# Kernel optimization log

Measured on AMD Instinct MI355X. Metric: run time of the kernel, lower is better.

Reference implementation:

```python
import jax, jax.numpy as jnp
import numpy as np

B, C, H, W = 2, 96, 40, 40
DIN, N, R, K = 192, 16, 6, 4  # d_inner, d_state, dt_rank, k_group


def silu(x):
    return x * jax.nn.sigmoid(x)


def dwconv3x3(x, w, b):
    # depthwise 3x3, SAME padding; w: (DIN,1,3,3)
    y = jax.lax.conv_general_dilated(x, w, (1, 1), [(1, 1), (1, 1)],
                                     feature_group_count=x.shape[1])
    return y + b[None, :, None, None]


def cross_scan(x):
    # (B,C,H,W) -> (B,4,C,L): row-major, col-major, and their reverses
    b, c, h, w = x.shape
    x0 = x.reshape(b, c, h * w)
    x1 = x.transpose(0, 1, 3, 2).reshape(b, c, h * w)
    return jnp.stack([x0, x1, x0[..., ::-1], x1[..., ::-1]], axis=1)


def cross_merge(y, h, w):
    # (B,4,C,H,W) -> (B,C,L)
    b, k, c = y.shape[0], y.shape[1], y.shape[2]
    y = y.reshape(b, k, c, h * w)
    y = y[:, :2] + y[:, 2:][..., ::-1]
    y1 = y[:, 1].reshape(b, c, w, h).transpose(0, 1, 3, 2).reshape(b, c, h * w)
    return y[:, 0] + y1


def selective_scan(u, dt, A, Bm, Cm, Dv, dbias):
    # u, dt: (B,K,DIN,L); A: (K*DIN,N); Bm, Cm: (B,K,N,L); Dv: (K*DIN,); dbias: (K*DIN,)
    b, k, d, l = u.shape
    n = A.shape[1]
    A4 = A.reshape(k, d, n)
    dt = jax.nn.softplus(dt + dbias.reshape(1, k, d, 1))
    # discretize: dA = exp(dt*A), dBu = dt*B*u  -> shapes (B,K,D,L,N)
    dA = jnp.exp(dt[..., None] * A4[None, :, :, None, :])
    dBu = dt[..., None] * Bm.transpose(0, 1, 3, 2)[:, :, None, :, :] * u[..., None]

    def combine(c1, c2):
        a1, b1 = c1
        a2, b2 = c2
        return a1 * a2, a2 * b1 + b2

    _, h = jax.lax.associative_scan(combine, (dA, dBu), axis=3)  # h: (B,K,D,L,N)
    y = jnp.einsum('bkdln,bknl->bkdl', h, Cm)
    return y + Dv.reshape(1, k, d, 1) * u


def ln2d(x, g, b):
    # LayerNorm over channel dim (channel_first LayerNorm2d)
    mu = x.mean(axis=1, keepdims=True)
    var = jnp.mean((x - mu) ** 2, axis=1, keepdims=True)
    xn = (x - mu) / jnp.sqrt(var + 1e-5)
    return xn * g[None, :, None, None] + b[None, :, None, None]


def setup_inputs():
    key = jax.random.key(0)
    ks = jax.random.split(key, 24)

    def rn(k, shape, s=0.02):
        return jax.random.normal(k, shape, dtype=jnp.float32) * s

    A_log = jnp.tile(jnp.log(jnp.arange(1, N + 1, dtype=jnp.float32))[None, :], (K * DIN, 1))
    return {
        'x_rgb': jax.random.normal(ks[0], (B, C, H, W), jnp.float32),
        'x_e': jax.random.normal(ks[1], (B, C, H, W), jnp.float32),
        'in_proj_w': rn(ks[2], (DIN, C)),
        'in_proj_mx_w': rn(ks[3], (DIN, C)),
        'conv_w': rn(ks[4], (DIN, 1, 3, 3), 0.1),
        'conv_b': jnp.zeros((DIN,), jnp.float32),
        'xproj1_w': rn(ks[5], (K, R + 2 * N, DIN)),
        'xproj2_w': rn(ks[6], (K, R + 2 * N, DIN)),
        'dtproj1_w': rn(ks[7], (K, DIN, R), 0.1),
        'dtproj1_b': rn(ks[8], (K, DIN), 0.1) - 4.0,
        'dtproj2_w': rn(ks[9], (K, DIN, R), 0.1),
        'dtproj2_b': rn(ks[10], (K, DIN), 0.1) - 4.0,
        'A_log_1': A_log,
        'A_log_2': A_log,
        'D_1': jnp.ones((K * DIN,), jnp.float32),
        'D_2': jnp.ones((K * DIN,), jnp.float32),
        'norm1_g': jnp.ones((DIN,), jnp.float32),
        'norm1_b': jnp.zeros((DIN,), jnp.float32),
        'norm2_g': jnp.ones((DIN,), jnp.float32),
        'norm2_b': jnp.zeros((DIN,), jnp.float32),
        'fc1_w1': rn(ks[11], (DIN // 16, DIN), 0.05),
        'fc1_w2': rn(ks[12], (DIN, DIN // 16), 0.05),
        'fc2_w1': rn(ks[13], (DIN // 16, DIN), 0.05),
        'fc2_w2': rn(ks[14], (DIN, DIN // 16), 0.05),
        'out_proj_w': rn(ks[15], (C, 2 * DIN)),
    }


def reference(x_rgb, x_e, in_proj_w, in_proj_mx_w, conv_w, conv_b, xproj1_w, xproj2_w,
              dtproj1_w, dtproj1_b, dtproj2_w, dtproj2_b, A_log_1, A_log_2, D_1, D_2,
              norm1_g, norm1_b, norm2_g, norm2_b, fc1_w1, fc1_w2, fc2_w1, fc2_w2, out_proj_w):
    # in_proj (1x1 conv style Linear2d)
    xr = jnp.einsum('oc,bchw->bohw', in_proj_w, x_rgb)
    xe = jnp.einsum('oc,bchw->bohw', in_proj_mx_w, x_e)
    # shared depthwise conv + SiLU
    xr = silu(dwconv3x3(xr, conv_w, conv_b))
    xe = silu(dwconv3x3(xe, conv_w, conv_b))
    b, d, h, w = xr.shape

    xs_r = cross_scan(xr)  # (B,K,DIN,L)
    xs_e = cross_scan(xe)

    def proj(xs, xp_w, dt_w):
        t = jnp.einsum('bkdl,kcd->bkcl', xs, xp_w)  # grouped 1x1 conv1d
        dts, Bm, Cm = jnp.split(t, [R, R + N], axis=2)
        dts = jnp.einsum('bkrl,kdr->bkdl', dts, dt_w)
        return dts, Bm, Cm

    d_r, B_r, C_r = proj(xs_r, xproj1_w, dtproj1_w)
    d_e, B_e, C_e = proj(xs_e, xproj2_w, dtproj2_w)

    # cross attention: rgb scan consumes C and D of the other modality
    y_r = selective_scan(xs_r, d_r, -jnp.exp(A_log_1), B_r, C_e, D_2, dtproj1_b.reshape(-1))
    y_e = selective_scan(xs_e, d_e, -jnp.exp(A_log_2), B_e, C_r, D_1, dtproj2_b.reshape(-1))

    y_r = cross_merge(y_r.reshape(b, K, d, h, w), h, w).reshape(b, d, h, w)
    y_e = cross_merge(y_e.reshape(b, K, d, h, w), h, w).reshape(b, d, h, w)
    y_r = ln2d(y_r, norm1_g, norm1_b)
    y_e = ln2d(y_e, norm2_g, norm2_b)

    # cross squeeze-excitation
    sq_r = xr.mean(axis=(2, 3))
    sq_e = xe.mean(axis=(2, 3))
    exc_r = jax.nn.sigmoid(silu(sq_r @ fc1_w1.T) @ fc1_w2.T)
    exc_e = jax.nn.sigmoid(silu(sq_e @ fc2_w1.T) @ fc2_w2.T)
    y_r = y_r * exc_e[:, :, None, None]
    y_e = y_e * exc_r[:, :, None, None]

    y = jnp.concatenate([y_r, y_e], axis=1)  # (B, 2*DIN, H, W)
    return jnp.einsum('oc,bchw->bohw', out_proj_w, y)
```

## Files before the change

kernel.cpp:

```cpp
#include <hip/hip_runtime.h>
#include <math.h>

#define BN   2
#define CIN  96
#define HH   40
#define WW   40
#define LL   1600
#define DIN  192
#define NS   16
#define RR   6
#define KK   4
#define CH   25

typedef _Float16 h16;

__device__ __forceinline__ float sigmoidf_(float x){ return 1.0f/(1.0f+expf(-x)); }
__device__ __forceinline__ float softplus_fast(float x){
  return x > 20.0f ? x : __logf(1.0f + __expf(x));
}

__device__ __forceinline__ void pow_tree(float R, float* p){
  float R2 = R * R;
  float R4 = R2 * R2;
  float R8 = R4 * R4;
  p[0]  = R;        p[1]  = R2;       p[2]  = R2 * R;   p[3]  = R4;
  p[4]  = R4 * R;   p[5]  = R4 * R2;  p[6]  = R4 * p[2];p[7]  = R8;
  p[8]  = R8 * R;   p[9]  = R8 * R2;  p[10] = R8 * p[2];p[11] = R8 * R4;
  p[12] = R8 * p[4];p[13] = R8 * p[5];p[14] = R8 * p[6];p[15] = R8 * R8;
}

__device__ __forceinline__ void unpack8(float4 v, float* dst){
  const h16* hp = reinterpret_cast<const h16*>(&v);
  #pragma unroll
  for (int i = 0; i < 8; ++i) dst[i] = (float)hp[i];
}

__global__ void k_inproj(const float* __restrict__ x_rgb, const float* __restrict__ x_e,
                         const float* __restrict__ w_rgb, const float* __restrict__ w_e,
                         float* __restrict__ xproj){
  __shared__ float xin[16][100];
  int l0 = blockIdx.x * 16;
  int mb = blockIdx.y;
  int m = mb / BN, b = mb % BN;
  const float* xsrc = (m == 0 ? x_rgb : x_e) + (size_t)b * CIN * LL;
  const float* w    = (m == 0 ? w_rgb : w_e);
  for (int idx = threadIdx.x; idx < CIN * 16; idx += 256){
    int c = idx >> 4, px = idx & 15;
    xin[px][c] = xsrc[c * LL + l0 + px];
  }
  __syncthreads();
  int px = threadIdx.x & 15;
  int o0 = (threadIdx.x >> 4) * 12;
  float acc[12];
  #pragma unroll
  for (int i = 0; i < 12; ++i) acc[i] = 0.f;
  const float4* xv = reinterpret_cast<const float4*>(xin[px]);
  for (int cc = 0; cc < CIN / 4; ++cc){
    float4 x4 = xv[cc];
    #pragma unroll
    for (int i = 0; i < 12; ++i){
      float4 w4 = *reinterpret_cast<const float4*>(w + (o0 + i) * CIN + cc * 4);
      acc[i] += w4.x * x4.x + w4.y * x4.y + w4.z * x4.z + w4.w * x4.w;
    }
  }
  #pragma unroll
  for (int i = 0; i < 12; ++i)
    xproj[((size_t)mb * DIN + o0 + i) * LL + l0 + px] = acc[i];
}

__global__ void k_conv(const float* __restrict__ xproj, const float* __restrict__ conv_w,
                       const float* __restrict__ conv_b, h16* __restrict__ x_act,
                       h16* __restrict__ x_actT, h16* __restrict__ u_chA,
                       h16* __restrict__ u_chT, float* __restrict__ sq){
  __shared__ float pl[LL];
  __shared__ float sact[LL + HH];
  __shared__ float red[4];
  int d  = blockIdx.x;
  int mb = blockIdx.y;
  const float* src = xproj + ((size_t)mb * DIN + d) * LL;
  for (int p = threadIdx.x; p < LL; p += blockDim.x) pl[p] = src[p];
  __syncthreads();
  float cw[9];
  #pragma unroll
  for (int j = 0; j < 9; ++j) cw[j] = conv_w[d * 9 + j];
  float bias = conv_b[d];
  h16* dst = x_act + ((size_t)mb * DIN + d) * LL;
  float lsum = 0.f;
  for (int p = threadIdx.x; p < LL; p += blockDim.x){
    int py = p / WW, px = p % WW;
    float acc = bias;
    #pragma unroll
    for (int dy = -1; dy <= 1; ++dy){
      int yy = py + dy;
      if (yy < 0 || yy >= HH) continue;
      #pragma unroll
      for (int dx = -1; dx <= 1; ++dx){
        int xx = px + dx;
        if (xx < 0 || xx >= WW) continue;
        acc += cw[(dy + 1) * 3 + (dx + 1)] * pl[yy * WW + xx];
      }
    }
    float s = acc * sigmoidf_(acc);
    dst[p] = (h16)s;
    sact[p + p / WW] = s;
    lsum += s;
  }
  #pragma unroll
  for (int off = 32; off; off >>= 1) lsum += __shfl_down(lsum, off);
  if ((threadIdx.x & 63) == 0) red[threadIdx.x >> 6] = lsum;
  __syncthreads();
  if (threadIdx.x == 0)
    sq[mb * DIN + d] = (red[0] + red[1] + red[2] + red[3]) * (1.0f / LL);
  size_t po = ((size_t)mb * DIN + d) * LL;
  h16* dstT = x_actT + po;
  h16* uA   = u_chA + po;
  h16* uT   = u_chT + po;
  for (int q = threadIdx.x; q < LL; q += blockDim.x){
    int lt = (q % WW) * WW + q / WW;
    dstT[q] = (h16)sact[lt + lt / WW];
    int l = (q & 63) * CH + (q >> 6);
    uA[q] = (h16)sact[l + l / WW];
    int pt = (l % WW) * WW + l / WW;
    uT[q] = (h16)sact[pt + pt / WW];
  }
}

__global__ void k_xproj(const h16* __restrict__ x_act, const h16* __restrict__ x_actT,
                        const float* __restrict__ xp1, const float* __restrict__ xp2,
                        float* __restrict__ tdt_ch, h16* __restrict__ B_ch,
                        h16* __restrict__ C_ch){
  int l0 = blockIdx.x * 64;
  int k  = blockIdx.y;
  int mb = blockIdx.z; int m = mb / BN;
  const float* xw = (m == 0 ? xp1 : xp2) + k * 38 * DIN;
  const h16* xa = ((k & 1) ? x_actT : x_act) + (size_t)mb * DIN * LL;
  bool rev = (k >= 2);
  int ll = threadIdx.x & 63;
  int g  = threadIdx.x >> 6;
  int c0 = g * 10;
  int l  = l0 + ll; if (rev) l = LL - 1 - l;
  const h16* xcol = xa + l;
  float acc[10];
  #pragma unroll
  for (int i = 0; i < 10; ++i) acc[i] = 0.f;
  if (g < 3){
    for (int dd = 0; dd < DIN; ++dd){
      float xv = (float)xcol[(size_t)dd * LL];
      #pragma unroll
      for (int i = 0; i < 10; ++i) acc[i] += xw[(c0 + i) * DIN + dd] * xv;
    }
  } else {
    for (int dd = 0; dd < DIN; ++dd){
      float xv = (float)xcol[(size_t)dd * LL];
      #pragma unroll
      for (int i = 0; i < 8; ++i) acc[i] += xw[(c0 + i) * DIN + dd] * xv;
    }
  }
  int mbk = mb * KK + k;
  int lq = l0 + ll;
  int q = (lq % CH) * 64 + lq / CH;
  int nc = (g < 3) ? 10 : 8;
  for (int i = 0; i < nc; ++i){
    int c = c0 + i;
    float v = acc[i];
    if (c < RR){
      tdt_ch[((size_t)mbk * RR + c) * LL + q] = v;
    } else if (c < RR + NS){
      int n = c - RR;
      B_ch[(((size_t)mbk * 2 + (n >> 3)) * LL + q) * 8 + (n & 7)] = (h16)v;
    } else {
      int n = c - RR - NS;
      C_ch[(((size_t)mbk * 2 + (n >> 3)) * LL + q) * 8 + (n & 7)] = (h16)v;
    }
  }
}

__global__ void __launch_bounds__(256, 4) k_scan(
    const h16* __restrict__ u_chA, const h16* __restrict__ u_chT,
    const float* __restrict__ tdt_all, const h16* __restrict__ B_ch,
    const h16* __restrict__ C_ch,
    const float* __restrict__ Alog1, const float* __restrict__ Alog2,
    const float* __restrict__ D1, const float* __restrict__ D2,
    const float* __restrict__ dtw1, const float* __restrict__ dtb1,
    const float* __restrict__ dtw2, const float* __restrict__ dtb2,
    h16* __restrict__ y_px){
  __shared__ h16 ysth[4][LL];
  __shared__ float dt_lds[4][LL];
  int wv   = threadIdx.x >> 6;
  int lane = threadIdx.x & 63;
  int chain = blockIdx.x * 4 + wv;
  int d   = chain % DIN;
  int mbk = chain / DIN;
  int k   = mbk % KK;
  int mb  = mbk / KK;
  int m = mb / BN, b = mb % BN;
  int kd = k * DIN + d;
  bool rev = (k >= 2);

  const float* Alog = (m == 0 ? Alog1 : Alog2) + kd * NS;
  float An[NS];
  bool fastA = true;
  #pragma unroll
  for (int n = 0; n < NS; ++n){
    An[n] = -__expf(Alog[n]);
    fastA = fastA && (fabsf(An[n] + (float)(n + 1)) <= 1e-4f * (float)(n + 1));
  }
  float Dv = (m == 0 ? D2 : D1)[kd];
  const float* dtw = (m == 0 ? dtw1 : dtw2) + kd * RR;
  float w0 = dtw[0], w1 = dtw[1], w2 = dtw[2], w3 = dtw[3], w4 = dtw[4], w5 = dtw[5];
  float dbias = (m == 0 ? dtb1 : dtb2)[kd];

  const float* t0 = tdt_all + (size_t)mbk * RR * LL;
  for (int s = 0; s < CH; ++s){
    int q = s * 64 + lane;
    float dtpre = w0 * t0[q] + w1 * t0[LL + q] + w2 * t0[2 * LL + q]
                + w3 * t0[3 * LL + q] + w4 * t0[4 * LL + q] + w5 * t0[5 * LL + q] + dbias;
    dt_lds[wv][q] = softplus_fast(dtpre);
  }

  const float4* B0 = reinterpret_cast<const float4*>(B_ch) + (size_t)mbk * 2 * LL;
  int mbk_o = ((1 - m) * BN + b) * KK + k;
  const float4* C0 = reinterpret_cast<const float4*>(C_ch) + (size_t)mbk_o * 2 * LL;
  const h16* urow = ((k & 1) ? u_chT : u_chA) + ((size_t)mb * DIN + d) * LL;

  float h[NS];
  #pragma unroll
  for (int n = 0; n < NS; ++n) h[n] = 0.f;
  float Sdt = 0.f;

  if (fastA){
    float4 bP0, bP1, cP0, cP1; float uP, dtP;
    {
      int q0 = lane;
      dtP = dt_lds[wv][q0];
      uP  = (float)urow[rev ? (LL - 1 - q0) : q0];
      bP0 = B0[q0]; bP1 = B0[LL + q0];
      cP0 = C0[q0]; cP1 = C0[LL + q0];
    }
    #pragma unroll 5
    for (int s = 0; s < CH; ++s){
      float dt = dtP, u = uP;
      float4 b0 = bP0, b1 = bP1, c0 = cP0, c1 = cP1;
      if (s + 1 < CH){
        int q1 = (s + 1) * 64 + lane;
        dtP = dt_lds[wv][q1];
        uP  = (float)urow[rev ? (LL - 1 - q1) : q1];
        bP0 = B0[q1]; bP1 = B0[LL + q1];
        cP0 = C0[q1]; cP1 = C0[LL + q1];
      }
      Sdt += dt;
      float du = dt * u;
      float Bv[NS], Cv[NS];
      unpack8(b0, Bv); unpack8(b1, Bv + 8);
      unpack8(c0, Cv); unpack8(c1, Cv + 8);
      float p[NS];
      pow_tree(__expf(-dt), p);
      float y0 = Dv * u, y1 = 0.f, y2 = 0.f, y3 = 0.f;
      #pragma unroll
      for (int n = 0; n < NS; ++n){
        h[n] = p[n] * h[n] + du * Bv[n];
        float t = h[n] * Cv[n];
        if      ((n & 3) == 0) y0 += t;
        else if ((n & 3) == 1) y1 += t;
        else if ((n & 3) == 2) y2 += t;
        else                   y3 += t;
      }
      ysth[wv][lane * CH + s] = (h16)((y0 + y1) + (y2 + y3));
    }
  } else {
    #pragma unroll 5
    for (int s = 0; s < CH; ++s){
      int q = s * 64 + lane;
      float dt = dt_lds[wv][q];
      Sdt += dt;
      float u  = (float)urow[rev ? (LL - 1 - q) : q];
      float du = dt * u;
      float Bv[NS], Cv[NS];
      unpack8(B0[q], Bv); unpack8(B0[LL + q], Bv + 8);
      unpack8(C0[q], Cv); unpack8(C0[LL + q], Cv + 8);
      float y0 = Dv * u, y1 = 0.f, y2 = 0.f, y3 = 0.f;
      #pragma unroll
      for (int n = 0; n < NS; ++n){
        float dA = __expf(dt * An[n]);
        h[n] = dA * h[n] + du * Bv[n];
        float t = h[n] * Cv[n];
        if      ((n & 3) == 0) y0 += t;
        else if ((n & 3) == 1) y1 += t;
        else if ((n & 3) == 2) y2 += t;
        else                   y3 += t;
      }
      ysth[wv][lane * CH + s] = (h16)((y0 + y1) + (y2 + y3));
    }
  }
  float aP[NS];
  if (fastA){
    pow_tree(__expf(-Sdt), aP);
  } else {
    #pragma unroll
    for (int n = 0; n < NS; ++n) aP[n] = __expf(Sdt * An[n]);
  }

  #pragma unroll
  for (int off = 1; off < 64; off <<= 1){
    #pragma unroll
    for (int n = 0; n < NS; ++n){
      float ap = __shfl_up(aP[n], off);
      float bp = __shfl_up(h[n],  off);
      if (lane >= off){
        h[n]  = aP[n] * bp + h[n];
        aP[n] = aP[n] * ap;
      }
    }
  }
  #pragma unroll
  for (int n = 0; n < NS; ++n){
    float v = __shfl_up(h[n], 1);
    h[n] = (lane == 0) ? 0.f : v;
  }

  if (fastA){
    float4 cP0, cP1; float dtP;
    {
      int q0 = lane;
      dtP = dt_lds[wv][q0];
      cP0 = C0[q0]; cP1 = C0[LL + q0];
    }
    float cum = 0.f;
    #pragma unroll 5
    for (int s = 0; s < CH; ++s){
      float dt = dtP;
      float4 c0 = cP0, c1 = cP1;
      if (s + 1 < CH){
        int q1 = (s + 1) * 64 + lane;
        dtP = dt_lds[wv][q1];
        cP0 = C0[q1]; cP1 = C0[LL + q1];
      }
      cum += dt;
      float Rc = __expf(-cum);
      float Cv[NS];
      unpack8(c0, Cv); unpack8(c1, Cv + 8);
      float p[NS];
      pow_tree(Rc, p);
      float s0 = 0.f, s1 = 0.f, s2 = 0.f, s3 = 0.f;
      #pragma unroll
      for (int n = 0; n < NS; ++n){
        float t = h[n] * p[n] * Cv[n];
        if      ((n & 3) == 0) s0 += t;
        else if ((n & 3) == 1) s1 += t;
        else if ((n & 3) == 2) s2 += t;
        else                   s3 += t;
      }
      int li = lane * CH + s;
      ysth[wv][li] = (h16)((float)ysth[wv][li] + (s0 + s1) + (s2 + s3));
    }
  } else {
    float cum = 0.f;
    #pragma unroll 5
    for (int s = 0; s < CH; ++s){
      int q = s * 64 + lane;
      cum += dt_lds[wv][q];
      float Cv[NS];
      unpack8(C0[q], Cv); unpack8(C0[LL + q], Cv + 8);
      float s0 = 0.f, s1 = 0.f, s2 = 0.f, s3 = 0.f;
      #pragma unroll
      for (int n = 0; n < NS; ++n){
        float t = h[n] * __expf(cum * An[n]) * Cv[n];
        if      ((n & 3) == 0) s0 += t;
        else if ((n & 3) == 1) s1 += t;
        else if ((n & 3) == 2) s2 += t;
        else                   s3 += t;
      }
      int li = lane * CH + s;
      ysth[wv][li] = (h16)((float)ysth[wv][li] + (s0 + s1) + (s2 + s3));
    }
  }

  h16* yo = y_px + (size_t)chain * LL;
  for (int qq = lane; qq < LL; qq += 64){
    int l;
    if      (k == 0) l = qq;
    else if (k == 1) l = (qq % WW) * WW + qq / WW;
    else if (k == 2) l = LL - 1 - qq;
    else             { int qt = (qq % WW) * WW + qq / WW; l = LL - 1 - qt; }
    yo[qq] = ysth[wv][l];
  }
}

__global__ void __launch_bounds__(256) k_mergeout(
    const h16* __restrict__ y_px, const float* __restrict__ sq,
    const float* __restrict__ fc1_w1, const float* __restrict__ fc1_w2,
    const float* __restrict__ fc2_w1, const float* __restrict__ fc2_w2,
    const float* __restrict__ n1g, const float* __restrict__ n1b,
    const float* __restrict__ n2g, const float* __restrict__ n2b,
    const float* __restrict__ wout, float* __restrict__ out){
  __shared__ float acc[2 * DIN][9];
  __shared__ float yt[8][388];
  __shared__ float ps[2][8][16], ps2[2][8][16];
  __shared__ float mu_s[2][8], inv_s[2][8];
  __shared__ float sqs[2][DIN];
  __shared__ float hid[2][12];
  __shared__ float exc_s[2][DIN];
  int p0 = blockIdx.x * 8;
  int b  = blockIdx.y;
  int tid = threadIdx.x;
  for (int idx = tid; idx < 2 * DIN * 8; idx += 256){
    int pp = idx & 7, row = idx >> 3;
    int mm = (row >= DIN), dd = row - mm * DIN;
    const h16* yb = y_px + ((size_t)(mm * BN + b) * KK * DIN + dd) * LL + p0 + pp;
    acc[row][pp] = (float)yb[0] + (float)yb[(size_t)DIN * LL]
                 + (float)yb[2 * (size_t)DIN * LL] + (float)yb[3 * (size_t)DIN * LL];
  }
  for (int i = tid; i < 2 * DIN; i += 256){
    int mm = (i >= DIN), dd = i - mm * DIN;
    sqs[mm][dd] = sq[((1 - mm) * BN + b) * DIN + dd];
  }
  __syncthreads();
  if (tid < 24){
    int mm = tid / 12, j = tid - mm * 12;
    const float* w1 = (mm == 1 ? fc1_w1 : fc2_w1);
    float a = 0.f;
    for (int cch = 0; cch < DIN; ++cch) a += w1[j * DIN + cch] * sqs[mm][cch];
    hid[mm][j] = a * sigmoidf_(a);
  }
  {
    int pp = tid & 7, mm = (tid >> 3) & 1, g = tid >> 4;
    float s = 0.f, s2 = 0.f;
    #pragma unroll 4
    for (int j = 0; j < 12; ++j){
      float v = acc[mm * DIN + g * 12 + j][pp];
      s += v; s2 += v * v;
    }
    ps[mm][pp][g] = s; ps2[mm][pp][g] = s2;
  }
  __syncthreads();
  if (tid < 16){
    int mm = tid >> 3, pp = tid & 7;
    float s = 0.f, s2 = 0.f;
    #pragma unroll
    for (int g = 0; g < 16; ++g){ s += ps[mm][pp][g]; s2 += ps2[mm][pp][g]; }
    float mu  = s * (1.0f / DIN);
    float var = s2 * (1.0f / DIN) - mu * mu;
    mu_s[mm][pp] = mu; inv_s[mm][pp] = rsqrtf(var + 1e-5f);
  }
  for (int i = tid; i < 2 * DIN; i += 256){
    int mm = (i >= DIN), dd = i - mm * DIN;
    const float* w2 = (mm == 1 ? fc1_w2 : fc2_w2);
    float e = 0.f;
    #pragma unroll
    for (int j = 0; j < 12; ++j) e += w2[dd * 12 + j] * hid[mm][j];
    exc_s[mm][dd] = sigmoidf_(e);
  }
  __syncthreads();
  for (int idx = tid; idx < 2 * DIN * 8; idx += 256){
    int pp = idx & 7, row = idx >> 3;
    int mm = (row >= DIN), dd = row - mm * DIN;
    float g  = (mm ? n2g : n1g)[dd];
    float bb = (mm ? n2b : n1b)[dd];
    float v = (acc[row][pp] - mu_s[mm][pp]) * inv_s[mm][pp] * g + bb;
    yt[pp][row] = v * exc_s[mm][dd];
  }
  __syncthreads();
  int pp = tid & 7;
  int o0 = (tid >> 3) * 3;
  float a3[3] = {0.f, 0.f, 0.f};
  const float4* yv = reinterpret_cast<const float4*>(yt[pp]);
  for (int cc = 0; cc < 96; ++cc){
    float4 x4 = yv[cc];
    #pragma unroll
    for (int i = 0; i < 3; ++i){
      float4 w4 = *reinterpret_cast<const float4*>(wout + (o0 + i) * 2 * DIN + cc * 4);
      a3[i] += w4.x * x4.x + w4.y * x4.y + w4.z * x4.z + w4.w * x4.w;
    }
  }
  #pragma unroll
  for (int i = 0; i < 3; ++i)
    out[((size_t)b * CIN + o0 + i) * LL + p0 + pp] = a3[i];
}

extern "C" void kernel_launch(void* const* d_in, const int* in_sizes, int n_in,
                              void* d_out, int out_size, void* d_ws, size_t ws_size,
                              hipStream_t stream){
  const float* x_rgb   = (const float*)d_in[0];
  const float* x_e     = (const float*)d_in[1];
  const float* in_w    = (const float*)d_in[2];
  const float* in_mx_w = (const float*)d_in[3];
  const float* conv_w  = (const float*)d_in[4];
  const float* conv_b  = (const float*)d_in[5];
  const float* xp1     = (const float*)d_in[6];
  const float* xp2     = (const float*)d_in[7];
  const float* dtw1    = (const float*)d_in[8];
  const float* dtb1    = (const float*)d_in[9];
  const float* dtw2    = (const float*)d_in[10];
  const float* dtb2    = (const float*)d_in[11];
  const float* Alog1   = (const float*)d_in[12];
  const float* Alog2   = (const float*)d_in[13];
  const float* D1      = (const float*)d_in[14];
  const float* D2      = (const float*)d_in[15];
  const float* n1g     = (const float*)d_in[16];
  const float* n1b     = (const float*)d_in[17];
  const float* n2g     = (const float*)d_in[18];
  const float* n2b     = (const float*)d_in[19];
  const float* fc1_w1  = (const float*)d_in[20];
  const float* fc1_w2  = (const float*)d_in[21];
  const float* fc2_w1  = (const float*)d_in[22];
  const float* fc2_w2  = (const float*)d_in[23];
  const float* wout    = (const float*)d_in[24];

  float* ws = (float*)d_ws;
  h16*   u_chA   = (h16*)(ws);
  h16*   u_chT   = (h16*)(ws + 1228800);
  h16*   x_act   = (h16*)(ws + 2457600);
  h16*   x_actT  = (h16*)(ws + 3686400);
  float* xproj   = ws + 4915200;
  h16*   y_px    = (h16*)(ws + 6144000);
  h16*   B_ch    = (h16*)(ws + 11059200);
  h16*   C_ch    = (h16*)(ws + 11468800);
  float* tdt_ch  = ws + 11878400;
  float* sq      = ws + 12032000;

  k_inproj  <<<dim3(LL / 16, 2 * BN), 256, 0, stream>>>(x_rgb, x_e, in_w, in_mx_w, xproj);
  k_conv    <<<dim3(DIN, 2 * BN), 256, 0, stream>>>(xproj, conv_w, conv_b,
                                                    x_act, x_actT, u_chA, u_chT, sq);
  k_xproj   <<<dim3(LL / 64, KK, 2 * BN), 256, 0, stream>>>(x_act, x_actT, xp1, xp2,
                                                            tdt_ch, B_ch, C_ch);
  k_scan    <<<768, 256, 0, stream>>>(u_chA, u_chT, tdt_ch, B_ch, C_ch,
                                      Alog1, Alog2, D1, D2,
                                      dtw1, dtb1, dtw2, dtb2, y_px);
  k_mergeout<<<dim3(LL / 8, BN), 256, 0, stream>>>(y_px, sq,
                                                   fc1_w1, fc1_w2, fc2_w1, fc2_w2,
                                                   n1g, n1b, n2g, n2b,
                                                   wout, (float*)d_out);
}
```

Before: 156.8 us.

## Move dt projection and softplus into xproj kernel, store fp16 dt for scan

The dt_rank-to-d_inner projection and softplus now run at the end of the xproj kernel: the six dt-rank values are staged in shared memory and a precomputed fp16 dt tensor is written per chain. The scan kernel reads dt straight from global memory instead of recomputing it into a 25 KB shared buffer, which cuts its LDS footprint and may raise occupancy. The cost is a larger global intermediate (DIN×L per mbk in fp16) and reduced dt precision. The workspace offsets are also repacked.

```diff
diff --git a/kernel.cpp b/kernel.cpp
--- a/kernel.cpp
+++ b/kernel.cpp
@@ -127,8 +127,11 @@
 
 __global__ void k_xproj(const h16* __restrict__ x_act, const h16* __restrict__ x_actT,
                         const float* __restrict__ xp1, const float* __restrict__ xp2,
-                        float* __restrict__ tdt_ch, h16* __restrict__ B_ch,
-                        h16* __restrict__ C_ch){
+                        const float* __restrict__ dtw1, const float* __restrict__ dtb1,
+                        const float* __restrict__ dtw2, const float* __restrict__ dtb2,
+                        h16* __restrict__ B_ch, h16* __restrict__ C_ch,
+                        h16* __restrict__ dsp_all){
+  __shared__ float td[RR][64];
   int l0 = blockIdx.x * 64;
   int k  = blockIdx.y;
   int mb = blockIdx.z; int m = mb / BN;
@@ -164,7 +167,7 @@
     int c = c0 + i;
     float v = acc[i];
     if (c < RR){
-      tdt_ch[((size_t)mbk * RR + c) * LL + q] = v;
+      td[c][ll] = v;
     } else if (c < RR + NS){
       int n = c - RR;
       B_ch[(((size_t)mbk * 2 + (n >> 3)) * LL + q) * 8 + (n & 7)] = (h16)v;
@@ -173,19 +176,31 @@
       C_ch[(((size_t)mbk * 2 + (n >> 3)) * LL + q) * 8 + (n & 7)] = (h16)v;
     }
   }
+  __syncthreads();
+  const float* dtw = (m == 0 ? dtw1 : dtw2);
+  const float* dtb = (m == 0 ? dtb1 : dtb2);
+  h16* dsp = dsp_all + (size_t)mbk * DIN * LL;
+  for (int idx = threadIdx.x; idx < DIN * 64; idx += 256){
+    int dd = idx >> 6, px = idx & 63;
+    int kd = k * DIN + dd;
+    const float* w = dtw + kd * RR;
+    float a = dtb[kd];
+    #pragma unroll
+    for (int r = 0; r < RR; ++r) a += w[r] * td[r][px];
+    int lq2 = l0 + px;
+    int q2 = (lq2 % CH) * 64 + lq2 / CH;
+    dsp[(size_t)dd * LL + q2] = (h16)softplus_fast(a);
+  }
 }
 
 __global__ void __launch_bounds__(256, 4) k_scan(
     const h16* __restrict__ u_chA, const h16* __restrict__ u_chT,
-    const float* __restrict__ tdt_all, const h16* __restrict__ B_ch,
+    const h16* __restrict__ dsp_all, const h16* __restrict__ B_ch,
     const h16* __restrict__ C_ch,
     const float* __restrict__ Alog1, const float* __restrict__ Alog2,
     const float* __restrict__ D1, const float* __restrict__ D2,
-    const float* __restrict__ dtw1, const float* __restrict__ dtb1,
-    const float* __restrict__ dtw2, const float* __restrict__ dtb2,
     h16* __restrict__ y_px){
   __shared__ h16 ysth[4][LL];
-  __shared__ float dt_lds[4][LL];
   int wv   = threadIdx.x >> 6;
   int lane = threadIdx.x & 63;
   int chain = blockIdx.x * 4 + wv;
@@ -206,18 +221,8 @@
     fastA = fastA && (fabsf(An[n] + (float)(n + 1)) <= 1e-4f * (float)(n + 1));
   }
   float Dv = (m == 0 ? D2 : D1)[kd];
-  const float* dtw = (m == 0 ? dtw1 : dtw2) + kd * RR;
-  float w0 = dtw[0], w1 = dtw[1], w2 = dtw[2], w3 = dtw[3], w4 = dtw[4], w5 = dtw[5];
-  float dbias = (m == 0 ? dtb1 : dtb2)[kd];
-
-  const float* t0 = tdt_all + (size_t)mbk * RR * LL;
-  for (int s = 0; s < CH; ++s){
-    int q = s * 64 + lane;
-    float dtpre = w0 * t0[q] + w1 * t0[LL + q] + w2 * t0[2 * LL + q]
-                + w3 * t0[3 * LL + q] + w4 * t0[4 * LL + q] + w5 * t0[5 * LL + q] + dbias;
-    dt_lds[wv][q] = softplus_fast(dtpre);
-  }
-
+
+  const h16* dsp = dsp_all + (size_t)chain * LL;
   const float4* B0 = reinterpret_cast<const float4*>(B_ch) + (size_t)mbk * 2 * LL;
   int mbk_o = ((1 - m) * BN + b) * KK + k;
   const float4* C0 = reinterpret_cast<const float4*>(C_ch) + (size_t)mbk_o * 2 * LL;
@@ -232,7 +237,7 @@
     float4 bP0, bP1, cP0, cP1; float uP, dtP;
     {
       int q0 = lane;
-      dtP = dt_lds[wv][q0];
+      dtP = (float)dsp[q0];
       uP  = (float)urow[rev ? (LL - 1 - q0) : q0];
       bP0 = B0[q0]; bP1 = B0[LL + q0];
       cP0 = C0[q0]; cP1 = C0[LL + q0];
@@ -243,7 +248,7 @@
       float4 b0 = bP0, b1 = bP1, c0 = cP0, c1 = cP1;
       if (s + 1 < CH){
         int q1 = (s + 1) * 64 + lane;
-        dtP = dt_lds[wv][q1];
+        dtP = (float)dsp[q1];
         uP  = (float)urow[rev ? (LL - 1 - q1) : q1];
         bP0 = B0[q1]; bP1 = B0[LL + q1];
         cP0 = C0[q1]; cP1 = C0[LL + q1];
@@ -271,7 +276,7 @@
     #pragma unroll 5
     for (int s = 0; s < CH; ++s){
       int q = s * 64 + lane;
-      float dt = dt_lds[wv][q];
+      float dt = (float)dsp[q];
       Sdt += dt;
       float u  = (float)urow[rev ? (LL - 1 - q) : q];
       float du = dt * u;
@@ -322,7 +327,7 @@
     float4 cP0, cP1; float dtP;
     {
       int q0 = lane;
-      dtP = dt_lds[wv][q0];
+      dtP = (float)dsp[q0];
       cP0 = C0[q0]; cP1 = C0[LL + q0];
     }
     float cum = 0.f;
@@ -332,7 +337,7 @@
       float4 c0 = cP0, c1 = cP1;
       if (s + 1 < CH){
         int q1 = (s + 1) * 64 + lane;
-        dtP = dt_lds[wv][q1];
+        dtP = (float)dsp[q1];
         cP0 = C0[q1]; cP1 = C0[LL + q1];
       }
       cum += dt;
@@ -358,7 +363,7 @@
     #pragma unroll 5
     for (int s = 0; s < CH; ++s){
       int q = s * 64 + lane;
-      cum += dt_lds[wv][q];
+      cum += (float)dsp[q];
       float Cv[NS];
       unpack8(C0[q], Cv); unpack8(C0[LL + q], Cv + 8);
       float s0 = 0.f, s1 = 0.f, s2 = 0.f, s3 = 0.f;
@@ -508,24 +513,24 @@
 
   float* ws = (float*)d_ws;
   h16*   u_chA   = (h16*)(ws);
-  h16*   u_chT   = (h16*)(ws + 1228800);
-  h16*   x_act   = (h16*)(ws + 2457600);
-  h16*   x_actT  = (h16*)(ws + 3686400);
-  float* xproj   = ws + 4915200;
-  h16*   y_px    = (h16*)(ws + 6144000);
-  h16*   B_ch    = (h16*)(ws + 11059200);
-  h16*   C_ch    = (h16*)(ws + 11468800);
-  float* tdt_ch  = ws + 11878400;
-  float* sq      = ws + 12032000;
+  h16*   u_chT   = (h16*)(ws + 614400);
+  h16*   x_act   = (h16*)(ws + 1228800);
+  h16*   x_actT  = (h16*)(ws + 1843200);
+  float* xproj   = ws + 2457600;
+  h16*   y_px    = (h16*)(ws + 3686400);
+  h16*   B_ch    = (h16*)(ws + 8601600);
+  h16*   C_ch    = (h16*)(ws + 8806400);
+  h16*   dsp     = (h16*)(ws + 9011200);
+  float* sq      = ws + 11468800;
 
   k_inproj  <<<dim3(LL / 16, 2 * BN), 256, 0, stream>>>(x_rgb, x_e, in_w, in_mx_w, xproj);
   k_conv    <<<dim3(DIN, 2 * BN), 256, 0, stream>>>(xproj, conv_w, conv_b,
                                                     x_act, x_actT, u_chA, u_chT, sq);
   k_xproj   <<<dim3(LL / 64, KK, 2 * BN), 256, 0, stream>>>(x_act, x_actT, xp1, xp2,
-                                                            tdt_ch, B_ch, C_ch);
-  k_scan    <<<768, 256, 0, stream>>>(u_chA, u_chT, tdt_ch, B_ch, C_ch,
-                                      Alog1, Alog2, D1, D2,
-                                      dtw1, dtb1, dtw2, dtb2, y_px);
+                                                            dtw1, dtb1, dtw2, dtb2,
+                                                            B_ch, C_ch, dsp);
+  k_scan    <<<768, 256, 0, stream>>>(u_chA, u_chT, dsp, B_ch, C_ch,
+                                      Alog1, Alog2, D1, D2, y_px);
   k_mergeout<<<dim3(LL / 8, BN), 256, 0, stream>>>(y_px, sq,
                                                    fc1_w1, fc1_w2, fc2_w1, fc2_w2,
                                                    n1g, n1b, n2g, n2b,
```

New measurement: 163.0 us. 1.04x slower.
